# Kernel optimization log

Hardware: AMD Instinct MI355X
Metric: run time of the kernel (lower is better)

Reference implementation:

```python
import jax, jax.numpy as jnp
import numpy as np


def setup_inputs() -> dict:
    key = jax.random.key(0)
    ks = jax.random.split(key, 7)
    B, NU, NI, F, L = 16384, 100000, 100000, 512, 256
    x = jax.random.randint(ks[0], (B, 2), 0, min(NU, NI), dtype=jnp.int64)
    user_lookup = jax.random.normal(ks[1], (NU, F), dtype=jnp.float32)
    item_lookup = jax.random.normal(ks[2], (NI, F), dtype=jnp.float32)
    s = 1.0 / np.sqrt(F)
    user_W = jax.random.normal(ks[3], (L, F), dtype=jnp.float32) * s
    user_b = jax.random.normal(ks[4], (L,), dtype=jnp.float32) * s
    item_W = jax.random.normal(ks[5], (L, F), dtype=jnp.float32) * s
    item_b = jax.random.normal(ks[6], (L,), dtype=jnp.float32) * s
    return {"x": x, "user_lookup": user_lookup, "item_lookup": item_lookup,
            "user_W": user_W, "user_b": user_b, "item_W": item_W, "item_b": item_b}


def _encode(feats, W, b):
    # Linear (torch weight layout [out, in]) + relu, the mDA encoder
    return jax.nn.relu(jnp.einsum('bf,lf->bl', feats, W) + b)


def reference(x, user_lookup, item_lookup, user_W, user_b, item_W, item_b):
    user_x = user_lookup[x[:, 0]]            # [B, F] gather
    item_x = item_lookup[x[:, 1]]            # [B, F] gather
    user_latent = _encode(user_x, user_W, user_b)   # [B, L]
    item_latent = _encode(item_x, item_W, item_b)   # [B, L]
    # diag(U @ I.T) == rowwise dot; same math, no [B,B] intermediate
    diagonal = jnp.sum(user_latent * item_latent, axis=-1)
    return diagonal[:, None]                 # [B, 1]
```

## Files before the change

kernel.cpp:

```cpp
#include <hip/hip_runtime.h>
#include <stdint.h>

#define B_TOTAL 16384
#define F 512
#define L 256
#define TB 32
#define KC 64
#define LDP 72

typedef _Float16 half8 __attribute__((ext_vector_type(8)));
typedef float floatx4 __attribute__((ext_vector_type(4)));

__device__ __align__(16) _Float16 g_wt[2][8][L][KC];

__global__ void wconv_kernel(const float* __restrict__ uW,
                             const float* __restrict__ iW) {
    int tid = blockIdx.x * blockDim.x + threadIdx.x;
    int which = tid >> 17;
    int r = tid & 131071;
    int f = r & 511;
    float v = which ? iW[r] : uW[r];
    g_wt[which][f >> 6][r >> 9][f & 63] = (_Float16)v;
}

__launch_bounds__(256, 2)
__global__ void fused_kernel(const int* __restrict__ x,
                             const float* __restrict__ ulook,
                             const float* __restrict__ ilook,
                             const float* __restrict__ ub,
                             const float* __restrict__ ib,
                             float* __restrict__ out) {
    __shared__ _Float16 sA[TB][LDP];
    __shared__ float    sRed[TB];
    __shared__ int      sIdx[2][TB];

    const int t = threadIdx.x;
    const int bbase = blockIdx.x * TB;

    if (t < 2 * TB) {
        int r = t >> 1, c = t & 1;
        sIdx[c][r] = x[(bbase + r) * 2 + c];
    }
    if (t < TB) sRed[t] = 0.0f;
    __syncthreads();

    const int wave = t >> 6;
    const int lane = t & 63;
    const int l15  = lane & 15;
    const int quad = lane >> 4;
    const int nbase = wave * 64;

    floatx4 ulat[2][4];
    floatx4 acc[2][4];

    const int arow = t >> 3;
    const int aoff = (t & 7) * 8;

    #pragma unroll 1
    for (int pass = 0; pass < 2; ++pass) {
        const float* __restrict__ look = pass ? ilook : ulook;
        const float* __restrict__ bias = pass ? ib : ub;

        #pragma unroll
        for (int mt = 0; mt < 2; ++mt)
            #pragma unroll
            for (int nt = 0; nt < 4; ++nt) {
                floatx4 z = {0.f, 0.f, 0.f, 0.f};
                acc[mt][nt] = z;
            }

        const int rowidx = sIdx[pass][arow];
        const float* asrc = look + (size_t)rowidx * F + aoff;

        float4 p0 = *(const float4*)(asrc);
        float4 p1 = *(const float4*)(asrc + 4);

        #pragma unroll 1
        for (int ks = 0; ks < 8; ++ks) {
            __syncthreads();

            {
                _Float16 h[8];
                h[0] = (_Float16)p0.x; h[1] = (_Float16)p0.y;
                h[2] = (_Float16)p0.z; h[3] = (_Float16)p0.w;
                h[4] = (_Float16)p1.x; h[5] = (_Float16)p1.y;
                h[6] = (_Float16)p1.z; h[7] = (_Float16)p1.w;
                *(half8*)(&sA[arow][aoff]) = *(half8*)h;
            }
            if (ks < 7) {
                const float* src = asrc + (ks + 1) * KC;
                p0 = *(const float4*)(src);
                p1 = *(const float4*)(src + 4);
            }
            __syncthreads();

            const _Float16* __restrict__ bb = &g_wt[pass][ks][0][0];
            half8 bfr[2][4];
            #pragma unroll
            for (int kt = 0; kt < 2; ++kt)
                #pragma unroll
                for (int nt = 0; nt < 4; ++nt)
                    bfr[kt][nt] = *(const half8*)(bb + (nbase + nt * 16 + l15) * KC
                                                     + kt * 32 + quad * 8);
            half8 af[2][2];
            #pragma unroll
            for (int kt = 0; kt < 2; ++kt)
                #pragma unroll
                for (int mt = 0; mt < 2; ++mt)
                    af[kt][mt] = *(const half8*)(&sA[mt * 16 + l15][kt * 32 + quad * 8]);

            #pragma unroll
            for (int kt = 0; kt < 2; ++kt)
                #pragma unroll
                for (int mt = 0; mt < 2; ++mt)
                    #pragma unroll
                    for (int nt = 0; nt < 4; ++nt)
                        acc[mt][nt] = __builtin_amdgcn_mfma_f32_16x16x32_f16(
                            af[kt][mt], bfr[kt][nt], acc[mt][nt], 0, 0, 0);
        }

        if (pass == 0) {
            #pragma unroll
            for (int mt = 0; mt < 2; ++mt)
                #pragma unroll
                for (int nt = 0; nt < 4; ++nt) {
                    int n = nbase + nt * 16 + l15;
                    float bv = bias[n];
                    #pragma unroll
                    for (int r = 0; r < 4; ++r) {
                        float v = acc[mt][nt][r] + bv;
                        ulat[mt][nt][r] = v > 0.f ? v : 0.f;
                    }
                }
        } else {
            #pragma unroll
            for (int mt = 0; mt < 2; ++mt) {
                float partial[4] = {0.f, 0.f, 0.f, 0.f};
                #pragma unroll
                for (int nt = 0; nt < 4; ++nt) {
                    int n = nbase + nt * 16 + l15;
                    float bv = bias[n];
                    #pragma unroll
                    for (int r = 0; r < 4; ++r) {
                        float v = acc[mt][nt][r] + bv;
                        v = v > 0.f ? v : 0.f;
                        partial[r] += v * ulat[mt][nt][r];
                    }
                }
                #pragma unroll
                for (int r = 0; r < 4; ++r) {
                    float v = partial[r];
                    v += __shfl_xor(v, 1);
                    v += __shfl_xor(v, 2);
                    v += __shfl_xor(v, 4);
                    v += __shfl_xor(v, 8);
                    if (l15 == 0)
                        atomicAdd(&sRed[mt * 16 + quad * 4 + r], v);
                }
            }
        }
    }

    __syncthreads();
    if (t < TB) out[bbase + t] = sRed[t];
}

extern "C" void kernel_launch(void* const* d_in, const int* in_sizes, int n_in,
                              void* d_out, int out_size, void* d_ws, size_t ws_size,
                              hipStream_t stream) {
    const int*   x     = (const int*)d_in[0];
    const float* ulook = (const float*)d_in[1];
    const float* ilook = (const float*)d_in[2];
    const float* uW    = (const float*)d_in[3];
    const float* ub    = (const float*)d_in[4];
    const float* iW    = (const float*)d_in[5];
    const float* ib    = (const float*)d_in[6];
    float* out = (float*)d_out;

    wconv_kernel<<<1024, 256, 0, stream>>>(uW, iW);
    fused_kernel<<<B_TOTAL / TB, 256, 0, stream>>>(x, ulook, ilook, ub, ib, out);
}
```

Baseline: 359.3 us.

## Load full user and item rows into shared memory upfront, remove per-step barriers

```diff
diff --git a/kernel.cpp b/kernel.cpp
--- a/kernel.cpp
+++ b/kernel.cpp
@@ -6,7 +6,7 @@
 #define L 256
 #define TB 32
 #define KC 64
-#define LDP 72
+#define LDA 520
 
 typedef _Float16 half8 __attribute__((ext_vector_type(8)));
 typedef float floatx4 __attribute__((ext_vector_type(4)));
@@ -30,35 +30,59 @@
                              const float* __restrict__ ub,
                              const float* __restrict__ ib,
                              float* __restrict__ out) {
-    __shared__ _Float16 sA[TB][LDP];
+    __shared__ _Float16 sA[2][TB][LDA];
     __shared__ float    sRed[TB];
-    __shared__ int      sIdx[2][TB];
 
     const int t = threadIdx.x;
     const int bbase = blockIdx.x * TB;
 
-    if (t < 2 * TB) {
-        int r = t >> 1, c = t & 1;
-        sIdx[c][r] = x[(bbase + r) * 2 + c];
+    if (t < TB) sRed[t] = 0.0f;
+
+    const int arow = t >> 3;
+    const int alane = t & 7;
+    const int rowu = x[(bbase + arow) * 2 + 0];
+    const int rowi = x[(bbase + arow) * 2 + 1];
+
+    {
+        const float* __restrict__ srcu = ulook + (size_t)rowu * F;
+        const float* __restrict__ srci = ilook + (size_t)rowi * F;
+        #pragma unroll
+        for (int c = 0; c < 8; ++c) {
+            int col = c * KC + alane * 8;
+            float4 v0 = *(const float4*)(srcu + col);
+            float4 v1 = *(const float4*)(srcu + col + 4);
+            _Float16 h[8];
+            h[0] = (_Float16)v0.x; h[1] = (_Float16)v0.y;
+            h[2] = (_Float16)v0.z; h[3] = (_Float16)v0.w;
+            h[4] = (_Float16)v1.x; h[5] = (_Float16)v1.y;
+            h[6] = (_Float16)v1.z; h[7] = (_Float16)v1.w;
+            *(half8*)(&sA[0][arow][col]) = *(half8*)h;
+        }
+        #pragma unroll
+        for (int c = 0; c < 8; ++c) {
+            int col = c * KC + alane * 8;
+            float4 v0 = *(const float4*)(srci + col);
+            float4 v1 = *(const float4*)(srci + col + 4);
+            _Float16 h[8];
+            h[0] = (_Float16)v0.x; h[1] = (_Float16)v0.y;
+            h[2] = (_Float16)v0.z; h[3] = (_Float16)v0.w;
+            h[4] = (_Float16)v1.x; h[5] = (_Float16)v1.y;
+            h[6] = (_Float16)v1.z; h[7] = (_Float16)v1.w;
+            *(half8*)(&sA[1][arow][col]) = *(half8*)h;
+        }
     }
-    if (t < TB) sRed[t] = 0.0f;
     __syncthreads();
 
-    const int wave = t >> 6;
     const int lane = t & 63;
     const int l15  = lane & 15;
     const int quad = lane >> 4;
-    const int nbase = wave * 64;
+    const int nbase = (t >> 6) * 64;
 
     floatx4 ulat[2][4];
     floatx4 acc[2][4];
 
-    const int arow = t >> 3;
-    const int aoff = (t & 7) * 8;
-
     #pragma unroll 1
     for (int pass = 0; pass < 2; ++pass) {
-        const float* __restrict__ look = pass ? ilook : ulook;
         const float* __restrict__ bias = pass ? ib : ub;
 
         #pragma unroll
@@ -69,31 +93,8 @@
                 acc[mt][nt] = z;
             }
 
-        const int rowidx = sIdx[pass][arow];
-        const float* asrc = look + (size_t)rowidx * F + aoff;
-
-        float4 p0 = *(const float4*)(asrc);
-        float4 p1 = *(const float4*)(asrc + 4);
-
-        #pragma unroll 1
+        #pragma unroll 2
         for (int ks = 0; ks < 8; ++ks) {
-            __syncthreads();
-
-            {
-                _Float16 h[8];
-                h[0] = (_Float16)p0.x; h[1] = (_Float16)p0.y;
-                h[2] = (_Float16)p0.z; h[3] = (_Float16)p0.w;
-                h[4] = (_Float16)p1.x; h[5] = (_Float16)p1.y;
-                h[6] = (_Float16)p1.z; h[7] = (_Float16)p1.w;
-                *(half8*)(&sA[arow][aoff]) = *(half8*)h;
-            }
-            if (ks < 7) {
-                const float* src = asrc + (ks + 1) * KC;
-                p0 = *(const float4*)(src);
-                p1 = *(const float4*)(src + 4);
-            }
-            __syncthreads();
-
             const _Float16* __restrict__ bb = &g_wt[pass][ks][0][0];
             half8 bfr[2][4];
             #pragma unroll
@@ -107,7 +108,8 @@
             for (int kt = 0; kt < 2; ++kt)
                 #pragma unroll
                 for (int mt = 0; mt < 2; ++mt)
-                    af[kt][mt] = *(const half8*)(&sA[mt * 16 + l15][kt * 32 + quad * 8]);
+                    af[kt][mt] = *(const half8*)(&sA[pass][mt * 16 + l15]
+                                                    [ks * KC + kt * 32 + quad * 8]);
 
             #pragma unroll
             for (int kt = 0; kt < 2; ++kt)
```

After: 363.8 us. About the same (+1.3%).
